# Performance work log

Measured on AMD Instinct MI355X. Metric: run time of the kernel, lower is better.

## Reference

```python
import jax, jax.numpy as jnp
import numpy as np
import math

B, S, E = 2, 2048, 1024
H = 16
D = E // H  # head dim = 64


def setup_inputs() -> dict:
    key = jax.random.key(0)
    ks = jax.random.split(key, 9)
    s = 1.0 / math.sqrt(E)
    return {
        "x": jax.random.normal(ks[0], (B, S, E), dtype=jnp.float32),
        "Wq": jax.random.uniform(ks[1], (E, E), jnp.float32, -s, s),
        "bq": jnp.zeros((E,), jnp.float32),
        "Wk": jax.random.uniform(ks[2], (E, E), jnp.float32, -s, s),
        "bk": jnp.zeros((E,), jnp.float32),
        "Wv": jax.random.uniform(ks[3], (E, E), jnp.float32, -s, s),
        "bv": jnp.zeros((E,), jnp.float32),
        "Wo": jax.random.uniform(ks[4], (E, E), jnp.float32, -s, s),
        "bo": jnp.zeros((E,), jnp.float32),
    }


def reference(x, Wq, bq, Wk, bk, Wv, bv, Wo, bo):
    b, s, e = x.shape
    q = x @ Wq + bq  # [B,S,E]
    k = x @ Wk + bk
    v = x @ Wv + bv
    # [B,S,E] -> [B,H,S,D]
    q = q.reshape(b, s, H, D).transpose(0, 2, 1, 3)
    k = k.reshape(b, s, H, D).transpose(0, 2, 1, 3)
    v = v.reshape(b, s, H, D).transpose(0, 2, 1, 3)
    scores = jnp.einsum('bhqd,bhkd->bhqk', q, k) / jnp.sqrt(jnp.float32(D))
    causal = jnp.tril(jnp.ones((s, s), dtype=bool))  # keep lower triangle
    scores = jnp.where(causal, scores, -jnp.inf)
    attn = jax.nn.softmax(scores, axis=-1)
    # dropout is identity in eval mode
    out = jnp.einsum('bhqk,bhkd->bhqd', attn, v)
    out = out.transpose(0, 2, 1, 3).reshape(b, s, e)
    return out @ Wo + bo
```

## Files before the change

### kernel.cpp

```cpp
#include <hip/hip_runtime.h>
#include <hip/hip_bf16.h>
#include <math.h>

#define B_ 2
#define S_ 2048
#define E_ 1024
#define H_ 16
#define D_ 64
#define M_ (B_*S_)

typedef __attribute__((ext_vector_type(8))) short short8v;
typedef __attribute__((ext_vector_type(4))) float floatx4;

__device__ __forceinline__ short f2bf(float f) {
    union { float f; unsigned u; } x; x.f = f;
    unsigned r = (x.u + 0x7fffu + ((x.u >> 16) & 1u)) >> 16;
    return (short)r;
}

__device__ __forceinline__ unsigned pk_bf16(float a, float b) {
    union { float f; unsigned u; } x, y;
    x.f = a; y.f = b;
    return __builtin_amdgcn_perm(y.u + 0x8000u, x.u + 0x8000u, 0x07060302u);
}

__device__ __forceinline__ float fast_exp2(float x) {
#if __has_builtin(__builtin_amdgcn_exp2f)
    return __builtin_amdgcn_exp2f(x);
#else
    return __expf(x * 0.6931471805599453f);
#endif
}

__device__ __forceinline__ void gl2lds16(const void* g, void* l) {
    __builtin_amdgcn_global_load_lds(
        (const __attribute__((address_space(1))) void*)g,
        (__attribute__((address_space(3))) void*)l, 16, 0, 0);
}

__device__ __forceinline__ int swz_off(int row, int cg) {
    return row*64 + (((cg ^ (row & 7)) & 7) << 3);
}

__global__ __launch_bounds__(256) void prep(
    const float* __restrict__ x, short* __restrict__ xb,
    const float* __restrict__ W0, const float* __restrict__ W1,
    const float* __restrict__ W2, const float* __restrict__ W3,
    short* __restrict__ T0, short* __restrict__ T1,
    short* __restrict__ T2, short* __restrict__ T3)
{
    const int bid = blockIdx.x;
    if (bid < 2048) {
        const size_t i = ((size_t)bid*256 + threadIdx.x) * 8;
        float4 a = *(const float4*)(x + i);
        float4 b = *(const float4*)(x + i + 4);
        int4 p = { (int)pk_bf16(a.x,a.y), (int)pk_bf16(a.z,a.w),
                   (int)pk_bf16(b.x,b.y), (int)pk_bf16(b.z,b.w) };
        *(int4*)(xb + i) = p;
        return;
    }
    const int tb = bid - 2048;
    const int z = tb >> 10;
    const float* W = (z==0)?W0:(z==1)?W1:(z==2)?W2:W3;
    short*       T = (z==0)?T0:(z==1)?T1:(z==2)?T2:T3;
    __shared__ float tile[32][33];
    const int k0 = ((tb>>5)&31)*32, n0 = (tb&31)*32;
    const int r = threadIdx.x >> 5, c = threadIdx.x & 31;
    #pragma unroll
    for (int i=0;i<4;i++)
        tile[r+8*i][c] = W[(size_t)(k0+r+8*i)*E_ + n0 + c];
    __syncthreads();
    #pragma unroll
    for (int i=0;i<4;i++)
        T[(size_t)(n0+r+8*i)*E_ + k0 + c] = f2bf(tile[c][r+8*i]);
}

__global__ __launch_bounds__(512, 2) void qkv_gemm(
    const short* __restrict__ xb, const short* __restrict__ Wt,
    const float* __restrict__ bq, const float* __restrict__ bk, const float* __restrict__ bv,
    short* __restrict__ Qo, short* __restrict__ Ko, short* __restrict__ Vo)
{
    __shared__ __align__(16) short As[2][256*64];
    __shared__ __align__(16) short Bs[2][256*64];

    const int t = threadIdx.x;
    const int wave = t >> 6, lane = t & 63;
    const int quad = lane >> 4, l15 = lane & 15;
    const int wr = wave >> 2, wc = wave & 3;

    const int bid = blockIdx.x;
    const int sw  = (bid & 7) * 24 + (bid >> 3);
    const int m0  = (sw / 12) * 256;
    const int nti = sw % 12;
    const int nf0 = nti * 256;
    const int z   = nf0 >> 10;
    const float* bb = (z==0) ? bq : (z==1) ? bk : bv;
    short* out      = (z==0) ? Qo : (z==1) ? Ko : Vo;
    const float sc  = (z==0) ? 0.18033688011112042f : 1.0f;

    const int sr8 = lane >> 3;
    const int scs = ((lane & 7) ^ sr8) * 8;

    const short* Ag = xb + (size_t)m0  * E_;
    const short* Bg = Wt + (size_t)nf0 * E_;

    floatx4 acc[8][4];
    #pragma unroll
    for (int i=0;i<8;i++)
        #pragma unroll
        for (int j=0;j<4;j++) acc[i][j] = (floatx4){0.f,0.f,0.f,0.f};

    auto stageA = [&](int p, int h, int kt) {
        const int rb = h*128 + wave*16;
        const short* src = Ag + (size_t)(rb + sr8)*E_ + kt*64 + scs;
        #pragma unroll
        for (int c=0;c<2;c++)
            gl2lds16(src + (size_t)c*8*E_, &As[p][(rb + c*8)*64]);
    };
    auto stageB = [&](int p, int h, int kt) {
        const int rb = h*128 + wave*16;
        const short* src = Bg + (size_t)(rb + sr8)*E_ + kt*64 + scs;
        #pragma unroll
        for (int c=0;c<2;c++)
            gl2lds16(src + (size_t)c*8*E_, &Bs[p][(rb + c*8)*64]);
    };

    short8v a[4][2], b[4][2];
    auto rdA = [&](int p, int row16, int ks) -> short8v {
        return *(const short8v*)&As[p][swz_off(wr*128 + row16*16 + l15, quad + ks*4)];
    };
    auto rdB = [&](int p, int row16, int ks) -> short8v {
        return *(const short8v*)&Bs[p][swz_off(wc*64  + row16*16 + l15, quad + ks*4)];
    };
    auto mm = [&](int mbase, int nbase) {
        #pragma unroll
        for (int mt=0;mt<4;mt++)
            #pragma unroll
            for (int nt=0;nt<2;nt++)
                #pragma unroll
                for (int ks=0;ks<2;ks++)
                    acc[mbase+mt][nbase+nt] = __builtin_amdgcn_mfma_f32_16x16x32_bf16(
                        a[mt][ks], b[nbase+nt][ks], acc[mbase+mt][nbase+nt], 0,0,0);
    };

    auto ktile = [&](int tt, int p) {
        #pragma unroll
        for (int mt=0;mt<4;mt++){ a[mt][0]=rdA(p,mt,0); a[mt][1]=rdA(p,mt,1); }
        #pragma unroll
        for (int nt=0;nt<2;nt++){ b[nt][0]=rdB(p,nt,0); b[nt][1]=rdB(p,nt,1); }
        __builtin_amdgcn_s_barrier();
        __builtin_amdgcn_s_setprio(1);
        mm(0,0);
        __builtin_amdgcn_s_setprio(0);
        __builtin_amdgcn_s_barrier();
        #pragma unroll
        for (int nt=2;nt<4;nt++){ b[nt][0]=rdB(p,nt,0); b[nt][1]=rdB(p,nt,1); }
        __builtin_amdgcn_s_barrier();
        __builtin_amdgcn_s_setprio(1);
        mm(0,2);
        __builtin_amdgcn_s_setprio(0);
        __builtin_amdgcn_s_barrier();
        #pragma unroll
        for (int mt=0;mt<4;mt++){ a[mt][0]=rdA(p,4+mt,0); a[mt][1]=rdA(p,4+mt,1); }
        if (tt+2 < 16) stageB(p, 0, tt+2);
        __builtin_amdgcn_s_barrier();
        __builtin_amdgcn_s_setprio(1);
        mm(4,0);
        __builtin_amdgcn_s_setprio(0);
        __builtin_amdgcn_s_barrier();
        if (tt+2 < 16) { stageB(p, 1, tt+2); stageA(p, 0, tt+2); stageA(p, 1, tt+2); }
        __builtin_amdgcn_s_barrier();
        __builtin_amdgcn_s_setprio(1);
        mm(4,2);
        __builtin_amdgcn_s_setprio(0);
        if (tt+2 < 16)      asm volatile("s_waitcnt vmcnt(8)" ::: "memory");
        else if (tt+1 < 16) asm volatile("s_waitcnt vmcnt(0)" ::: "memory");
        __builtin_amdgcn_s_barrier();
    };

    stageA(0,0,0); stageA(0,1,0); stageB(0,0,0); stageB(0,1,0);
    stageA(1,0,1); stageA(1,1,1); stageB(1,0,1); stageB(1,1,1);
    asm volatile("s_waitcnt vmcnt(8)" ::: "memory");
    __builtin_amdgcn_s_barrier();

    #pragma unroll 1
    for (int tb = 0; tb < 16; tb += 2) {
        ktile(tb,   0);
        ktile(tb+1, 1);
    }

    #pragma unroll
    for (int nt=0;nt<4;nt++) {
        const int nw = (nf0 & 1023) + wc*64 + nt*16 + l15;
        const float bias = bb[nw];
        const int h = nw >> 6, d = nw & 63;
        #pragma unroll
        for (int mt=0;mt<8;mt++) {
            #pragma unroll
            for (int r=0;r<4;r++) {
                const int m = m0 + wr*128 + mt*16 + quad*4 + r;
                const int b2 = m >> 11, s = m & (S_-1);
                const int bh = (b2<<4) + h;
                const float v = (acc[mt][nt][r] + bias) * sc;
                if (z == 0) {
                    out[((size_t)bh*S_ + s)*D_ + d] = f2bf(v);
                } else if (z == 1) {
                    const int ts = s >> 6, kk = s & 63;
                    const int c = kk*8 + ((d>>3) ^ ((kk>>2)&7));
                    out[((size_t)bh*32 + ts)*4096 + c*8 + (d&7)] = f2bf(v);
                } else {
                    const int ts = s >> 6, sk = s & 63;
                    const int c = d*8 + ((sk>>3) ^ (d&7));
                    out[((size_t)bh*32 + ts)*4096 + c*8 + (sk&7)] = f2bf(v);
                }
            }
        }
    }
}

__global__ __launch_bounds__(256, 1) void attn_kernel(
    const short* __restrict__ Q, const short* __restrict__ K, const short* __restrict__ V,
    short* __restrict__ AO)
{
    const int bh = blockIdx.x;
    const int qb = (gridDim.y - 1 - blockIdx.y) * 128;
    const int t = threadIdx.x;
    const int wave = t >> 6, lane = t & 63;
    const int quad = lane >> 4, l15 = lane & 15;

    const short* Qp = Q + (size_t)bh * (S_*D_);
    const short* Kp = K + (size_t)bh * (S_*D_);
    const short* Vp = V + (size_t)bh * (S_*D_);

    __shared__ __align__(16) short KVs[2][8192];
    __shared__ __align__(16) short Psl[2][4][2][16*72];

    const int qA = qb + wave*16;
    const int qB = qb + 64 + wave*16;
    const short* qa = Qp + (size_t)(qA + l15)*D_ + quad*8;
    const short8v qA0 = *(const short8v*)qa, qA1 = *(const short8v*)(qa + 32);
    const short* qbp = Qp + (size_t)(qB + l15)*D_ + quad*8;
    const short8v qB0 = *(const short8v*)qbp, qB1 = *(const short8v*)(qbp + 32);

    const int qrbA = qA + quad*4;
    const int qrbB = qB + quad*4;

    floatx4 oA[4], oB[4];
    #pragma unroll
    for (int i=0;i<4;i++) { oA[i] = (floatx4){0,0,0,0}; oB[i] = (floatx4){0,0,0,0}; }
    float tsA[4] = {0,0,0,0}, tsB[4] = {0,0,0,0};

    const int L = (qb >> 6) + 2;
    const int swz = l15 & 7;

    auto stage = [&](int kt, int p) {
        const short* src = ((wave < 2) ? Kp : Vp) + (size_t)kt*4096 + (wave&1)*2048 + lane*8;
        short* dst = &KVs[p][((wave < 2) ? 0 : 4096) + (wave&1)*2048];
        #pragma unroll
        for (int c=0;c<4;c++)
            gl2lds16(src + c*512, dst + c*512);
    };
    auto qk2 = [&](const short* KL, floatx4 (&sA)[4], floatx4 (&sB)[4]) {
        __builtin_amdgcn_s_setprio(1);
        #pragma unroll
        for (int h=0; h<4; h++) {
            const int rowc = (4*l15 + h)*8;
            short8v b0 = *(const short8v*)(KL + (rowc + (quad       ^ swz))*8);
            short8v b1 = *(const short8v*)(KL + (rowc + ((4 + quad) ^ swz))*8);
            sA[h] = (floatx4){0.f,0.f,0.f,0.f};
            sA[h] = __builtin_amdgcn_mfma_f32_16x16x32_bf16(qA0, b0, sA[h], 0,0,0);
            sA[h] = __builtin_amdgcn_mfma_f32_16x16x32_bf16(qA1, b1, sA[h], 0,0,0);
            sB[h] = (floatx4){0.f,0.f,0.f,0.f};
            sB[h] = __builtin_amdgcn_mfma_f32_16x16x32_bf16(qB0, b0, sB[h], 0,0,0);
            sB[h] = __builtin_amdgcn_mfma_f32_16x16x32_bf16(qB1, b1, sB[h], 0,0,0);
        }
        __builtin_amdgcn_s_setprio(0);
    };
    auto soft_u = [&](floatx4 (&s)[4], float* ts, short* pw, int qrb, int k0) {
        const int kk = k0 + 4*l15;
        #pragma unroll
        for (int r=0; r<4; r++) {
            const int qr = qrb + r;
            float p[4];
            #pragma unroll
            for (int h=0; h<4; h++) {
                const float e = fast_exp2(s[h][r]);
                p[h] = (kk + h > qr) ? 0.f : e;
            }
            ts[r] += (p[0] + p[1]) + (p[2] + p[3]);
            int2 pkv = { (int)pk_bf16(p[0], p[1]), (int)pk_bf16(p[2], p[3]) };
            *(int2*)(pw + (quad*4 + r)*72 + l15*4) = pkv;
        }
    };
    short8v vr[4][2];
    auto loadv = [&](const short* VL) {
        #pragma unroll
        for (int dt=0; dt<4; dt++) {
            const int rowc = (dt*16 + l15)*8;
            vr[dt][0] = *(const short8v*)(VL + (rowc + (quad       ^ swz))*8);
            vr[dt][1] = *(const short8v*)(VL + (rowc + ((4 + quad) ^ swz))*8);
        }
    };
    auto pv = [&](const short* pw, floatx4 (&o)[4]) {
        const short8v pf0 = *(const short8v*)(pw + l15*72 + quad*8);
        const short8v pf1 = *(const short8v*)(pw + l15*72 + 32 + quad*8);
        __builtin_amdgcn_s_setprio(1);
        #pragma unroll
        for (int dt=0; dt<4; dt++) {
            o[dt] = __builtin_amdgcn_mfma_f32_16x16x32_bf16(pf0, vr[dt][0], o[dt], 0,0,0);
            o[dt] = __builtin_amdgcn_mfma_f32_16x16x32_bf16(pf1, vr[dt][1], o[dt], 0,0,0);
        }
        __builtin_amdgcn_s_setprio(0);
    };

    stage(0, 0);
    __syncthreads();
    stage(1, 1);
    {
        floatx4 sA[4], sB[4];
        qk2(&KVs[0][0], sA, sB);
        loadv(&KVs[0][4096]);
        soft_u(sA, tsA, &Psl[0][wave][0][0], qrbA, 0);
        soft_u(sB, tsB, &Psl[0][wave][1][0], qrbB, 0);
    }

    for (int kt = 1; kt < L; kt++) {
        const int p = kt & 1;
        __syncthreads();
        if (kt + 1 < L) stage(kt + 1, p ^ 1);
        floatx4 sA[4], sB[4];
        qk2(&KVs[p][0], sA, sB);
        pv(&Psl[p^1][wave][0][0], oA);
        pv(&Psl[p^1][wave][1][0], oB);
        loadv(&KVs[p][4096]);
        const int k0 = kt << 6;
        soft_u(sA, tsA, &Psl[p][wave][0][0], qrbA, k0);
        soft_u(sB, tsB, &Psl[p][wave][1][0], qrbB, k0);
    }

    pv(&Psl[1][wave][0][0], oA);
    pv(&Psl[1][wave][1][0], oB);

    float lA[4], lB[4];
    #pragma unroll
    for (int r=0; r<4; r++) {
        float a = tsA[r], b = tsB[r];
        #pragma unroll
        for (int off=1; off<16; off<<=1) {
            a += __shfl_xor(a, off);
            b += __shfl_xor(b, off);
        }
        lA[r] = a; lB[r] = b;
    }

    const int b = bh >> 4, h = bh & 15;
    #pragma unroll
    for (int dt=0; dt<4; dt++) {
        #pragma unroll
        for (int r=0; r<4; r++) {
            const int d = dt*16 + l15;
            const int sA_ = qA + quad*4 + r;
            const int sB_ = qB + quad*4 + r;
            AO[((size_t)(b*S_ + sA_)*H_ + h)*D_ + d] = f2bf(oA[dt][r] / lA[r]);
            AO[((size_t)(b*S_ + sB_)*H_ + h)*D_ + d] = f2bf(oB[dt][r] / lB[r]);
        }
    }
}

__global__ __launch_bounds__(256) void out_gemm(
    const short* __restrict__ A, const short* __restrict__ Wto,
    const float* __restrict__ bo, float* __restrict__ out)
{
    __shared__ __align__(16) short As[128*64];
    __shared__ __align__(16) short Bs[64*64];

    const int t = threadIdx.x;
    const int wave = t >> 6, lane = t & 63;
    const int quad = lane >> 4, l15 = lane & 15;
    const int lin = blockIdx.x;
    const int m0 = (lin & 31) * 128;
    const int n0 = (lin >> 5) * 64;
    const int sr8 = lane >> 3;
    const int scs = ((lane & 7) ^ sr8) * 8;

    floatx4 acc[2][4];
    #pragma unroll
    for (int i=0;i<2;i++)
        #pragma unroll
        for (int j=0;j<4;j++) acc[i][j] = (floatx4){0.f,0.f,0.f,0.f};

    for (int k0 = 0; k0 < E_; k0 += 64) {
        #pragma unroll
        for (int c=0;c<4;c++) {
            const int rb = wave*32 + c*8;
            gl2lds16(A + (size_t)(m0+rb+sr8)*E_ + k0 + scs, &As[rb*64]);
        }
        #pragma unroll
        for (int c=0;c<2;c++) {
            const int rb = wave*16 + c*8;
            gl2lds16(Wto + (size_t)(n0+rb+sr8)*E_ + k0 + scs, &Bs[rb*64]);
        }
        __syncthreads();
        #pragma unroll
        for (int ks=0; ks<2; ks++) {
            const int cg = quad + ks*4;
            short8v a[2], b[4];
            #pragma unroll
            for (int mt=0;mt<2;mt++) a[mt] = *(const short8v*)&As[swz_off(wave*32+mt*16+l15, cg)];
            #pragma unroll
            for (int nt=0;nt<4;nt++) b[nt] = *(const short8v*)&Bs[swz_off(nt*16+l15, cg)];
            #pragma unroll
            for (int mt=0;mt<2;mt++)
                #pragma unroll
                for (int nt=0;nt<4;nt++)
                    acc[mt][nt] = __builtin_amdgcn_mfma_f32_16x16x32_bf16(a[mt], b[nt], acc[mt][nt], 0,0,0);
        }
        __syncthreads();
    }

    #pragma unroll
    for (int nt=0;nt<4;nt++) {
        const int n = n0 + nt*16 + l15;
        const float bias = bo[n];
        #pragma unroll
        for (int mt=0;mt<2;mt++) {
            #pragma unroll
            for (int r=0;r<4;r++) {
                const int m = m0 + wave*32 + mt*16 + quad*4 + r;
                out[(size_t)m*E_ + n] = acc[mt][nt][r] + bias;
            }
        }
    }
}

extern "C" void kernel_launch(void* const* d_in, const int* in_sizes, int n_in,
                              void* d_out, int out_size, void* d_ws, size_t ws_size,
                              hipStream_t stream)
{
    const float* x  = (const float*)d_in[0];
    const float* Wq = (const float*)d_in[1];
    const float* bq = (const float*)d_in[2];
    const float* Wk = (const float*)d_in[3];
    const float* bk = (const float*)d_in[4];
    const float* Wv = (const float*)d_in[5];
    const float* bv = (const float*)d_in[6];
    const float* Wo = (const float*)d_in[7];
    const float* bo = (const float*)d_in[8];

    short* xb  = (short*)d_ws;
    short* Tq  = xb  + (size_t)M_ * E_;
    short* Tk  = Tq  + (size_t)E_ * E_;
    short* Tv  = Tk  + (size_t)E_ * E_;
    short* To  = Tv  + (size_t)E_ * E_;
    short* Qw  = To  + (size_t)E_ * E_;
    short* Kw  = Qw  + (size_t)M_ * E_;
    short* Vw  = Kw  + (size_t)M_ * E_;
    short* AOw = Vw  + (size_t)M_ * E_;

    dim3 blk(256);
    prep<<<dim3(2048 + 4096), blk, 0, stream>>>(x, xb, Wq, Wk, Wv, Wo, Tq, Tk, Tv, To);
    qkv_gemm<<<dim3(192), dim3(512), 0, stream>>>(xb, Tq, bq, bk, bv, Qw, Kw, Vw);
    attn_kernel<<<dim3(B_*H_, S_/128), blk, 0, stream>>>(Qw, Kw, Vw, AOw);
    out_gemm<<<dim3(512), blk, 0, stream>>>(AOw, To, bo, (float*)d_out);
}
```

Measured before the change: 197.3 us.

## Retile QKV GEMM to 256x192 tiles so 256 blocks fill all CUs

```diff
diff --git a/kernel.cpp b/kernel.cpp
--- a/kernel.cpp
+++ b/kernel.cpp
@@ -81,7 +81,7 @@
     short* __restrict__ Qo, short* __restrict__ Ko, short* __restrict__ Vo)
 {
     __shared__ __align__(16) short As[2][256*64];
-    __shared__ __align__(16) short Bs[2][256*64];
+    __shared__ __align__(16) short Bs[2][192*64];
 
     const int t = threadIdx.x;
     const int wave = t >> 6, lane = t & 63;
@@ -89,14 +89,9 @@
     const int wr = wave >> 2, wc = wave & 3;
 
     const int bid = blockIdx.x;
-    const int sw  = (bid & 7) * 24 + (bid >> 3);
-    const int m0  = (sw / 12) * 256;
-    const int nti = sw % 12;
-    const int nf0 = nti * 256;
-    const int z   = nf0 >> 10;
-    const float* bb = (z==0) ? bq : (z==1) ? bk : bv;
-    short* out      = (z==0) ? Qo : (z==1) ? Ko : Vo;
-    const float sc  = (z==0) ? 0.18033688011112042f : 1.0f;
+    const int sw  = (bid & 7) * 32 + (bid >> 3);
+    const int m0  = (sw >> 4) * 256;
+    const int nf0 = (sw & 15) * 192;
 
     const int sr8 = lane >> 3;
     const int scs = ((lane & 7) ^ sr8) * 8;
@@ -104,11 +99,11 @@
     const short* Ag = xb + (size_t)m0  * E_;
     const short* Bg = Wt + (size_t)nf0 * E_;
 
-    floatx4 acc[8][4];
+    floatx4 acc[8][3];
     #pragma unroll
     for (int i=0;i<8;i++)
         #pragma unroll
-        for (int j=0;j<4;j++) acc[i][j] = (floatx4){0.f,0.f,0.f,0.f};
+        for (int j=0;j<3;j++) acc[i][j] = (floatx4){0.f,0.f,0.f,0.f};
 
     auto stageA = [&](int p, int h, int kt) {
         const int rb = h*128 + wave*16;
@@ -117,70 +112,76 @@
         for (int c=0;c<2;c++)
             gl2lds16(src + (size_t)c*8*E_, &As[p][(rb + c*8)*64]);
     };
-    auto stageB = [&](int p, int h, int kt) {
-        const int rb = h*128 + wave*16;
-        const short* src = Bg + (size_t)(rb + sr8)*E_ + kt*64 + scs;
-        #pragma unroll
-        for (int c=0;c<2;c++)
-            gl2lds16(src + (size_t)c*8*E_, &Bs[p][(rb + c*8)*64]);
-    };
-
-    short8v a[4][2], b[4][2];
+    auto stageB = [&](int p, int u, int kt) {
+        const int rb = u*64 + wave*8;
+        gl2lds16(Bg + (size_t)(rb + sr8)*E_ + kt*64 + scs, &Bs[p][rb*64]);
+    };
+
+    short8v a[2][2], b[3][2];
     auto rdA = [&](int p, int row16, int ks) -> short8v {
         return *(const short8v*)&As[p][swz_off(wr*128 + row16*16 + l15, quad + ks*4)];
     };
     auto rdB = [&](int p, int row16, int ks) -> short8v {
-        return *(const short8v*)&Bs[p][swz_off(wc*64  + row16*16 + l15, quad + ks*4)];
-    };
-    auto mm = [&](int mbase, int nbase) {
-        #pragma unroll
-        for (int mt=0;mt<4;mt++)
-            #pragma unroll
-            for (int nt=0;nt<2;nt++)
+        return *(const short8v*)&Bs[p][swz_off(wc*48 + row16*16 + l15, quad + ks*4)];
+    };
+    auto lda2 = [&](int p, int mbase) {
+        #pragma unroll
+        for (int j=0;j<2;j++)
+            #pragma unroll
+            for (int ks=0;ks<2;ks++) a[j][ks] = rdA(p, mbase+j, ks);
+    };
+    auto mm = [&](int mbase) {
+        #pragma unroll
+        for (int j=0;j<2;j++)
+            #pragma unroll
+            for (int nt=0;nt<3;nt++)
                 #pragma unroll
                 for (int ks=0;ks<2;ks++)
-                    acc[mbase+mt][nbase+nt] = __builtin_amdgcn_mfma_f32_16x16x32_bf16(
-                        a[mt][ks], b[nbase+nt][ks], acc[mbase+mt][nbase+nt], 0,0,0);
+                    acc[mbase+j][nt] = __builtin_amdgcn_mfma_f32_16x16x32_bf16(
+                        a[j][ks], b[nt][ks], acc[mbase+j][nt], 0,0,0);
     };
 
     auto ktile = [&](int tt, int p) {
         #pragma unroll
-        for (int mt=0;mt<4;mt++){ a[mt][0]=rdA(p,mt,0); a[mt][1]=rdA(p,mt,1); }
-        #pragma unroll
-        for (int nt=0;nt<2;nt++){ b[nt][0]=rdB(p,nt,0); b[nt][1]=rdB(p,nt,1); }
-        __builtin_amdgcn_s_barrier();
-        __builtin_amdgcn_s_setprio(1);
-        mm(0,0);
-        __builtin_amdgcn_s_setprio(0);
-        __builtin_amdgcn_s_barrier();
-        #pragma unroll
-        for (int nt=2;nt<4;nt++){ b[nt][0]=rdB(p,nt,0); b[nt][1]=rdB(p,nt,1); }
-        __builtin_amdgcn_s_barrier();
-        __builtin_amdgcn_s_setprio(1);
-        mm(0,2);
-        __builtin_amdgcn_s_setprio(0);
-        __builtin_amdgcn_s_barrier();
-        #pragma unroll
-        for (int mt=0;mt<4;mt++){ a[mt][0]=rdA(p,4+mt,0); a[mt][1]=rdA(p,4+mt,1); }
-        if (tt+2 < 16) stageB(p, 0, tt+2);
-        __builtin_amdgcn_s_barrier();
-        __builtin_amdgcn_s_setprio(1);
-        mm(4,0);
-        __builtin_amdgcn_s_setprio(0);
-        __builtin_amdgcn_s_barrier();
-        if (tt+2 < 16) { stageB(p, 1, tt+2); stageA(p, 0, tt+2); stageA(p, 1, tt+2); }
-        __builtin_amdgcn_s_barrier();
-        __builtin_amdgcn_s_setprio(1);
-        mm(4,2);
-        __builtin_amdgcn_s_setprio(0);
-        if (tt+2 < 16)      asm volatile("s_waitcnt vmcnt(8)" ::: "memory");
+        for (int nt=0;nt<3;nt++)
+            #pragma unroll
+            for (int ks=0;ks<2;ks++) b[nt][ks] = rdB(p, nt, ks);
+        lda2(p, 0);
+        if (tt+1 < 16) stageA(p^1, 0, tt+1);
+        __builtin_amdgcn_s_barrier();
+        __builtin_amdgcn_s_setprio(1);
+        mm(0);
+        __builtin_amdgcn_s_setprio(0);
+        __builtin_amdgcn_s_barrier();
+        lda2(p, 2);
+        if (tt+1 < 16) stageA(p^1, 1, tt+1);
+        __builtin_amdgcn_s_barrier();
+        __builtin_amdgcn_s_setprio(1);
+        mm(2);
+        __builtin_amdgcn_s_setprio(0);
+        __builtin_amdgcn_s_barrier();
+        lda2(p, 4);
+        if (tt+2 < 16) { stageB(p, 0, tt+2); stageB(p, 1, tt+2); }
+        __builtin_amdgcn_s_barrier();
+        __builtin_amdgcn_s_setprio(1);
+        mm(4);
+        __builtin_amdgcn_s_setprio(0);
+        __builtin_amdgcn_s_barrier();
+        lda2(p, 6);
+        if (tt+2 < 16) stageB(p, 2, tt+2);
+        __builtin_amdgcn_s_barrier();
+        __builtin_amdgcn_s_setprio(1);
+        mm(6);
+        __builtin_amdgcn_s_setprio(0);
+        if (tt+2 < 16)      asm volatile("s_waitcnt vmcnt(3)" ::: "memory");
         else if (tt+1 < 16) asm volatile("s_waitcnt vmcnt(0)" ::: "memory");
         __builtin_amdgcn_s_barrier();
     };
 
-    stageA(0,0,0); stageA(0,1,0); stageB(0,0,0); stageB(0,1,0);
-    stageA(1,0,1); stageA(1,1,1); stageB(1,0,1); stageB(1,1,1);
-    asm volatile("s_waitcnt vmcnt(8)" ::: "memory");
+    stageA(0,0,0); stageA(0,1,0);
+    stageB(0,0,0); stageB(0,1,0); stageB(0,2,0);
+    stageB(1,0,1); stageB(1,1,1); stageB(1,2,1);
+    asm volatile("s_waitcnt vmcnt(3)" ::: "memory");
     __builtin_amdgcn_s_barrier();
 
     #pragma unroll 1
@@ -190,10 +191,15 @@
     }
 
     #pragma unroll
-    for (int nt=0;nt<4;nt++) {
-        const int nw = (nf0 & 1023) + wc*64 + nt*16 + l15;
-        const float bias = bb[nw];
-        const int h = nw >> 6, d = nw & 63;
+    for (int nt=0;nt<3;nt++) {
+        const int nwg = nf0 + wc*48 + nt*16 + l15;
+        const int zf  = nwg >> 10;
+        const float* bbf = (zf==0) ? bq : (zf==1) ? bk : bv;
+        short* outf      = (zf==0) ? Qo : (zf==1) ? Ko : Vo;
+        const float scf  = (zf==0) ? 0.18033688011112042f : 1.0f;
+        const int nl = nwg & 1023;
+        const float bias = bbf[nl];
+        const int h = nl >> 6, d = nl & 63;
         #pragma unroll
         for (int mt=0;mt<8;mt++) {
             #pragma unroll
@@ -201,17 +207,17 @@
                 const int m = m0 + wr*128 + mt*16 + quad*4 + r;
                 const int b2 = m >> 11, s = m & (S_-1);
                 const int bh = (b2<<4) + h;
-                const float v = (acc[mt][nt][r] + bias) * sc;
-                if (z == 0) {
-                    out[((size_t)bh*S_ + s)*D_ + d] = f2bf(v);
-                } else if (z == 1) {
+                const float v = (acc[mt][nt][r] + bias) * scf;
+                if (zf == 0) {
+                    outf[((size_t)bh*S_ + s)*D_ + d] = f2bf(v);
+                } else if (zf == 1) {
                     const int ts = s >> 6, kk = s & 63;
                     const int c = kk*8 + ((d>>3) ^ ((kk>>2)&7));
-                    out[((size_t)bh*32 + ts)*4096 + c*8 + (d&7)] = f2bf(v);
+                    outf[((size_t)bh*32 + ts)*4096 + c*8 + (d&7)] = f2bf(v);
                 } else {
                     const int ts = s >> 6, sk = s & 63;
                     const int c = d*8 + ((sk>>3) ^ (d&7));
-                    out[((size_t)bh*32 + ts)*4096 + c*8 + (sk&7)] = f2bf(v);
+                    outf[((size_t)bh*32 + ts)*4096 + c*8 + (sk&7)] = f2bf(v);
                 }
             }
         }
@@ -459,7 +465,7 @@
 
     dim3 blk(256);
     prep<<<dim3(2048 + 4096), blk, 0, stream>>>(x, xb, Wq, Wk, Wv, Wo, Tq, Tk, Tv, To);
-    qkv_gemm<<<dim3(192), dim3(512), 0, stream>>>(xb, Tq, bq, bk, bv, Qw, Kw, Vw);
+    qkv_gemm<<<dim3(256), dim3(512), 0, stream>>>(xb, Tq, bq, bk, bv, Qw, Kw, Vw);
     attn_kernel<<<dim3(B_*H_, S_/128), blk, 0, stream>>>(Qw, Kw, Vw, AOw);
     out_gemm<<<dim3(512), blk, 0, stream>>>(AOw, To, bo, (float*)d_out);
 }
```

New measurement: 187.6 us. 1.05x faster.
